# Optimization experiments

Measured on AMD Instinct MI355X. Metric: run time of the kernel, lower is better.

## Reference

```python
import jax, jax.numpy as jnp
import numpy as np

DIM = 4096
N_HEADS = 32
N_KV_HEADS = 8
HEAD_DIM = DIM // N_HEADS  # 128
N_REP = N_HEADS // N_KV_HEADS  # 4
MAX_BS = 16
MAX_SEQ = 4096
SEQLEN = 1
START_POS = 4095
ROPE_THETA = 500000.0


def setup_inputs() -> dict:
    key = jax.random.key(0)
    ks = jax.random.split(key, 8)
    w_scale = 0.02  # keep logits in a sane range
    x = jax.random.normal(ks[0], (MAX_BS, SEQLEN, DIM), dtype=jnp.float32)
    wq = jax.random.normal(ks[1], (DIM, N_HEADS * HEAD_DIM), dtype=jnp.float32) * w_scale
    wk = jax.random.normal(ks[2], (DIM, N_KV_HEADS * HEAD_DIM), dtype=jnp.float32) * w_scale
    wv = jax.random.normal(ks[3], (DIM, N_KV_HEADS * HEAD_DIM), dtype=jnp.float32) * w_scale
    wo = jax.random.normal(ks[4], (N_HEADS * HEAD_DIM, DIM), dtype=jnp.float32) * w_scale
    cache_k = jax.random.normal(ks[5], (MAX_BS, MAX_SEQ, N_KV_HEADS, HEAD_DIM), dtype=jnp.float32)
    cache_v = jax.random.normal(ks[6], (MAX_BS, MAX_SEQ, N_KV_HEADS, HEAD_DIM), dtype=jnp.float32)
    # true rotary frequencies for positions [START_POS, START_POS+SEQLEN)
    inv_freq = 1.0 / (ROPE_THETA ** (np.arange(0, HEAD_DIM, 2, dtype=np.float32) / HEAD_DIM))  # [hd/2]
    t = np.arange(START_POS, START_POS + SEQLEN, dtype=np.float32)[:, None]  # [s,1]
    angles = t * inv_freq[None, :]  # [s, hd/2]
    freqs_cos = jnp.asarray(np.cos(angles), dtype=jnp.float32)
    freqs_sin = jnp.asarray(np.sin(angles), dtype=jnp.float32)
    return {"x": x, "wq": wq, "wk": wk, "wv": wv, "wo": wo,
            "cache_k": cache_k, "cache_v": cache_v,
            "freqs_cos": freqs_cos, "freqs_sin": freqs_sin,
            "start_pos": START_POS}


def _rope(t, cos, sin):
    # t: [b, s, h, hd]; cos/sin: [s, hd/2] -> broadcast [1, s, 1, hd/2]
    b, s, h, hd = t.shape
    tp = t.reshape(b, s, h, hd // 2, 2)
    e, o = tp[..., 0], tp[..., 1]
    c = cos[None, :, None, :]
    sn = sin[None, :, None, :]
    re = e * c - o * sn
    im = e * sn + o * c
    return jnp.stack([re, im], axis=-1).reshape(b, s, h, hd)


def reference(x, wq, wk, wv, wo, cache_k, cache_v, freqs_cos, freqs_sin, start_pos):
    bsz, seqlen, _ = x.shape
    xq = (x @ wq).reshape(bsz, seqlen, N_HEADS, HEAD_DIM)
    xk = (x @ wk).reshape(bsz, seqlen, N_KV_HEADS, HEAD_DIM)
    xv = (x @ wv).reshape(bsz, seqlen, N_KV_HEADS, HEAD_DIM)
    xq = _rope(xq, freqs_cos, freqs_sin)
    xk = _rope(xk, freqs_cos, freqs_sin)
    # KV-cache append
    cache_k = jax.lax.dynamic_update_slice(cache_k, xk, (0, start_pos, 0, 0))
    cache_v = jax.lax.dynamic_update_slice(cache_v, xv, (0, start_pos, 0, 0))
    kv_len = start_pos + seqlen  # static Python int
    keys = cache_k[:, :kv_len]    # [b, t, g, hd]
    values = cache_v[:, :kv_len]  # [b, t, g, hd]
    # GQA via broadcasting (math-equivalent to repeat_kv)
    q = xq.reshape(bsz, seqlen, N_KV_HEADS, N_REP, HEAD_DIM)
    scale = 1.0 / jnp.sqrt(jnp.float32(HEAD_DIM))
    scores = jnp.einsum('bsgrh,btgh->bgrst', q, keys) * scale  # [b,g,r,s,t]
    probs = jax.nn.softmax(scores.astype(jnp.float32), axis=-1).astype(xq.dtype)
    out = jnp.einsum('bgrst,btgh->bsgrh', probs, values)  # [b,s,g,r,hd]
    out = out.reshape(bsz, seqlen, N_HEADS * HEAD_DIM)
    return out @ wo
```

## Files before the change

### kernel.cpp

```cpp
#include <hip/hip_runtime.h>
#include <math.h>

#define DIM    4096
#define NH     32
#define NKV    8
#define HD     128
#define BS     16
#define KVLEN  4096
#define LASTPOS 4095
#define QKV_COLS 6144

#define WS_QKV   0
#define WS_ATTN  98304
#define WS_PART  163840

__global__ __launch_bounds__(256) void qkv_proj(
    const float* __restrict__ x, const float* __restrict__ wq,
    const float* __restrict__ wk, const float* __restrict__ wv,
    float* __restrict__ qkv) {
  __shared__ float xs[16 * 128];
  const int tid = threadIdx.x;
  const int col = (blockIdx.x * 256 + tid) * 2;
  const int k0 = blockIdx.y * 128;

  for (int i = tid; i < 2048; i += 256) {
    int b = i >> 7, k = i & 127;
    xs[i] = x[b * DIM + k0 + k];
  }
  __syncthreads();

  const float* w;
  int wstride, wcol;
  if (col < 4096)      { w = wq; wstride = 4096; wcol = col; }
  else if (col < 5120) { w = wk; wstride = 1024; wcol = col - 4096; }
  else                 { w = wv; wstride = 1024; wcol = col - 5120; }
  const float* wp = w + (size_t)k0 * wstride + wcol;

  float acc0[16], acc1[16];
#pragma unroll
  for (int b = 0; b < 16; ++b) { acc0[b] = 0.f; acc1[b] = 0.f; }

  for (int k = 0; k < 128; k += 4) {
    float2 w0 = *(const float2*)(wp + (size_t)(k + 0) * wstride);
    float2 w1 = *(const float2*)(wp + (size_t)(k + 1) * wstride);
    float2 w2 = *(const float2*)(wp + (size_t)(k + 2) * wstride);
    float2 w3 = *(const float2*)(wp + (size_t)(k + 3) * wstride);
#pragma unroll
    for (int b = 0; b < 16; ++b) {
      float4 xb = *(const float4*)(&xs[b * 128 + k]);
      acc0[b] += xb.x * w0.x + xb.y * w1.x + xb.z * w2.x + xb.w * w3.x;
      acc1[b] += xb.x * w0.y + xb.y * w1.y + xb.z * w2.y + xb.w * w3.y;
    }
  }
#pragma unroll
  for (int b = 0; b < 16; ++b) {
    atomicAdd(&qkv[b * QKV_COLS + col],     acc0[b]);
    atomicAdd(&qkv[b * QKV_COLS + col + 1], acc1[b]);
  }
}

__global__ __launch_bounds__(256) void rope_kernel(
    float* __restrict__ qkv, const float* __restrict__ fc,
    const float* __restrict__ fs) {
  int t = blockIdx.x * 256 + threadIdx.x;
  if (t >= 16 * 40 * 64) return;
  int i  = t & 63;
  int hh = (t >> 6) % 40;
  int b  = t / (40 * 64);
  float c = fc[i], s = fs[i];
  int base;
  float scale;
  if (hh < 32) { base = b * QKV_COLS + hh * 128 + 2 * i; scale = 0.08838834764831845f; }
  else         { base = b * QKV_COLS + 4096 + (hh - 32) * 128 + 2 * i; scale = 1.0f; }
  float e = qkv[base], o = qkv[base + 1];
  qkv[base]     = (e * c - o * s) * scale;
  qkv[base + 1] = (e * s + o * c) * scale;
}

__global__ __launch_bounds__(512, 4) void attn_partial(
    const float* __restrict__ cache_k, const float* __restrict__ cache_v,
    const float* __restrict__ qkv, float* __restrict__ part) {
  __shared__ float qs[512];
  __shared__ float ss[4 * 512];
  __shared__ float pacc[8][4][128];
  const int tid = threadIdx.x;
  const int w = tid >> 6, lane = tid & 63;
  const int p = lane >> 4, ql = lane & 15;
  const int chunk = blockIdx.x & 7;
  const int bg = blockIdx.x >> 3;
  const int b = bg >> 3, g = bg & 7;

  qs[tid & 511] = qkv[b * QKV_COLS + g * 512 + (tid & 511)];
  __syncthreads();

  float4 qA[4], qB[4];
#pragma unroll
  for (int h = 0; h < 4; ++h) {
    qA[h] = *(const float4*)(&qs[h * 128 + ql * 8]);
    qB[h] = *(const float4*)(&qs[h * 128 + ql * 8 + 4]);
  }

  const int t0 = chunk * 512;
  const float* kbase = cache_k + ((size_t)b * 4096 * 8 + g) * 128;
  const float* xk    = qkv + b * QKV_COLS + 4096 + g * 128;

  for (int it = 0; it < 16; ++it) {
    int r = w * 64 + it * 4 + p;
    int t = t0 + r;
    const float* krow = (t == LASTPOS) ? xk : (kbase + (size_t)t * 1024);
    float4 k0 = *(const float4*)(krow + ql * 8);
    float4 k1 = *(const float4*)(krow + ql * 8 + 4);
    float s[4];
#pragma unroll
    for (int h = 0; h < 4; ++h) {
      s[h] = k0.x * qA[h].x + k0.y * qA[h].y + k0.z * qA[h].z + k0.w * qA[h].w
           + k1.x * qB[h].x + k1.y * qB[h].y + k1.z * qB[h].z + k1.w * qB[h].w;
    }
#pragma unroll
    for (int off = 1; off < 16; off <<= 1) {
#pragma unroll
      for (int h = 0; h < 4; ++h) s[h] += __shfl_xor(s[h], off);
    }
    float v = (ql == 0) ? s[0] : (ql == 1) ? s[1] : (ql == 2) ? s[2] : s[3];
    if (ql < 4) ss[ql * 512 + r] = v;
  }
  __syncthreads();

  float* prow = part + ((size_t)(bg * 8 + chunk) * 4 + (w & 3)) * 130;
  if (w < 4) {
    float vals[8];
    float m = -1e30f;
#pragma unroll
    for (int i = 0; i < 8; ++i) {
      vals[i] = ss[w * 512 + lane + 64 * i];
      m = fmaxf(m, vals[i]);
    }
#pragma unroll
    for (int off = 1; off < 64; off <<= 1) m = fmaxf(m, __shfl_xor(m, off));
    float l = 0.f;
#pragma unroll
    for (int i = 0; i < 8; ++i) {
      float pe = __expf(vals[i] - m);
      ss[w * 512 + lane + 64 * i] = pe;
      l += pe;
    }
#pragma unroll
    for (int off = 1; off < 64; off <<= 1) l += __shfl_xor(l, off);
    if (lane == 0) { prow[128] = m; prow[129] = l; }
  }
  __syncthreads();

  const float* vbase = cache_v + ((size_t)b * 4096 * 8 + g) * 128;
  const float* xv    = qkv + b * QKV_COLS + 5120 + g * 128;
  float ax[4] = {0.f, 0.f, 0.f, 0.f}, ay[4] = {0.f, 0.f, 0.f, 0.f};
  for (int j = 0; j < 64; ++j) {
    int r = w * 64 + j;
    int t = t0 + r;
    const float* vrow = (t == LASTPOS) ? xv : (vbase + (size_t)t * 1024);
    float2 vv = ((const float2*)vrow)[lane];
    float p0 = ss[0 * 512 + r];
    float p1 = ss[1 * 512 + r];
    float p2 = ss[2 * 512 + r];
    float p3 = ss[3 * 512 + r];
    ax[0] += p0 * vv.x; ay[0] += p0 * vv.y;
    ax[1] += p1 * vv.x; ay[1] += p1 * vv.y;
    ax[2] += p2 * vv.x; ay[2] += p2 * vv.y;
    ax[3] += p3 * vv.x; ay[3] += p3 * vv.y;
  }
#pragma unroll
  for (int h = 0; h < 4; ++h) {
    pacc[w][h][2 * lane]     = ax[h];
    pacc[w][h][2 * lane + 1] = ay[h];
  }
  __syncthreads();

  {
    int h = tid >> 7, d = tid & 127;
    float sum = 0.f;
#pragma unroll
    for (int w2 = 0; w2 < 8; ++w2) sum += pacc[w2][h][d];
    part[((size_t)(bg * 8 + chunk) * 4 + h) * 130 + d] = sum;
  }
}

__global__ __launch_bounds__(256) void attn_combine(
    const float* __restrict__ part, float* __restrict__ attn_out) {
  int t = blockIdx.x * 256 + threadIdx.x;
  int d = t & 127, r = (t >> 7) & 3, bg = t >> 9;
  int b = bg >> 3, g = bg & 7;
  float ms[8];
  float M = -1e30f;
#pragma unroll
  for (int c = 0; c < 8; ++c) {
    ms[c] = part[((size_t)(bg * 8 + c) * 4 + r) * 130 + 128];
    M = fmaxf(M, ms[c]);
  }
  float num = 0.f, den = 0.f;
#pragma unroll
  for (int c = 0; c < 8; ++c) {
    const float* prow = part + ((size_t)(bg * 8 + c) * 4 + r) * 130;
    float wgt = __expf(ms[c] - M);
    num += wgt * prow[d];
    den += wgt * prow[129];
  }
  attn_out[b * DIM + (g * 4 + r) * 128 + d] = num / den;
}

__global__ __launch_bounds__(256) void out_proj(
    const float* __restrict__ attn, const float* __restrict__ wo,
    float* __restrict__ out) {
  __shared__ float xs[16 * 128];
  const int tid = threadIdx.x;
  const int col = (blockIdx.x * 256 + tid) * 2;
  const int k0 = blockIdx.y * 128;

  for (int i = tid; i < 2048; i += 256) {
    int b = i >> 7, k = i & 127;
    xs[i] = attn[b * DIM + k0 + k];
  }
  __syncthreads();

  const float* wp = wo + (size_t)k0 * 4096 + col;
  float acc0[16], acc1[16];
#pragma unroll
  for (int b = 0; b < 16; ++b) { acc0[b] = 0.f; acc1[b] = 0.f; }

  for (int k = 0; k < 128; k += 4) {
    float2 w0 = *(const float2*)(wp + (size_t)(k + 0) * 4096);
    float2 w1 = *(const float2*)(wp + (size_t)(k + 1) * 4096);
    float2 w2 = *(const float2*)(wp + (size_t)(k + 2) * 4096);
    float2 w3 = *(const float2*)(wp + (size_t)(k + 3) * 4096);
#pragma unroll
    for (int b = 0; b < 16; ++b) {
      float4 xb = *(const float4*)(&xs[b * 128 + k]);
      acc0[b] += xb.x * w0.x + xb.y * w1.x + xb.z * w2.x + xb.w * w3.x;
      acc1[b] += xb.x * w0.y + xb.y * w1.y + xb.z * w2.y + xb.w * w3.y;
    }
  }
#pragma unroll
  for (int b = 0; b < 16; ++b) {
    atomicAdd(&out[b * DIM + col],     acc0[b]);
    atomicAdd(&out[b * DIM + col + 1], acc1[b]);
  }
}

extern "C" void kernel_launch(void* const* d_in, const int* in_sizes, int n_in,
                              void* d_out, int out_size, void* d_ws, size_t ws_size,
                              hipStream_t stream) {
  const float* x  = (const float*)d_in[0];
  const float* wq = (const float*)d_in[1];
  const float* wk = (const float*)d_in[2];
  const float* wv = (const float*)d_in[3];
  const float* wo = (const float*)d_in[4];
  const float* ck = (const float*)d_in[5];
  const float* cv = (const float*)d_in[6];
  const float* fc = (const float*)d_in[7];
  const float* fs = (const float*)d_in[8];

  float* ws_f  = (float*)d_ws;
  float* qkv   = ws_f + WS_QKV;
  float* attn  = ws_f + WS_ATTN;
  float* part  = ws_f + WS_PART;
  float* out   = (float*)d_out;

  hipMemsetAsync(qkv, 0, 98304 * sizeof(float), stream);
  hipMemsetAsync(out, 0, 65536 * sizeof(float), stream);

  qkv_proj<<<dim3(12, 32), 256, 0, stream>>>(x, wq, wk, wv, qkv);
  rope_kernel<<<160, 256, 0, stream>>>(qkv, fc, fs);
  attn_partial<<<1024, 512, 0, stream>>>(ck, cv, qkv, part);
  attn_combine<<<256, 256, 0, stream>>>(part, attn);
  out_proj<<<dim3(8, 32), 256, 0, stream>>>(attn, wo, out);
}
```

Before: 202.3 us.

## Split GEMV K-dimension finer, widen V loads, pad score smem, fuse memsets

The QKV and output projections now split K into 64-wide slices, doubling the block count, and the output projection gives each thread one column instead of two. This raises parallelism for the weight-streaming GEMVs at the cost of twice as many atomicAdds. In attention, the P·V loop loads float4 V rows with two rows per wave iteration and reduces halves via shuffle, and the score buffer gets a padded stride to avoid LDS bank conflicts. The two hipMemsetAsync calls are replaced by a single zeroing kernel.

```diff
diff --git a/kernel.cpp b/kernel.cpp
--- a/kernel.cpp
+++ b/kernel.cpp
@@ -9,22 +9,31 @@
 #define KVLEN  4096
 #define LASTPOS 4095
 #define QKV_COLS 6144
+#define SS_STR 520
 
 #define WS_QKV   0
 #define WS_ATTN  98304
 #define WS_PART  163840
+
+__global__ __launch_bounds__(256) void zero_ws(
+    float* __restrict__ qkv, float* __restrict__ out) {
+  int i = blockIdx.x * 256 + threadIdx.x;
+  float4 z = make_float4(0.f, 0.f, 0.f, 0.f);
+  if (i < 24576) ((float4*)qkv)[i] = z;
+  else           ((float4*)out)[i - 24576] = z;
+}
 
 __global__ __launch_bounds__(256) void qkv_proj(
     const float* __restrict__ x, const float* __restrict__ wq,
     const float* __restrict__ wk, const float* __restrict__ wv,
     float* __restrict__ qkv) {
-  __shared__ float xs[16 * 128];
+  __shared__ float xs[16 * 64];
   const int tid = threadIdx.x;
   const int col = (blockIdx.x * 256 + tid) * 2;
-  const int k0 = blockIdx.y * 128;
-
-  for (int i = tid; i < 2048; i += 256) {
-    int b = i >> 7, k = i & 127;
+  const int k0 = blockIdx.y * 64;
+
+  for (int i = tid; i < 1024; i += 256) {
+    int b = i >> 6, k = i & 63;
     xs[i] = x[b * DIM + k0 + k];
   }
   __syncthreads();
@@ -40,14 +49,15 @@
 #pragma unroll
   for (int b = 0; b < 16; ++b) { acc0[b] = 0.f; acc1[b] = 0.f; }
 
-  for (int k = 0; k < 128; k += 4) {
+#pragma unroll 2
+  for (int k = 0; k < 64; k += 4) {
     float2 w0 = *(const float2*)(wp + (size_t)(k + 0) * wstride);
     float2 w1 = *(const float2*)(wp + (size_t)(k + 1) * wstride);
     float2 w2 = *(const float2*)(wp + (size_t)(k + 2) * wstride);
     float2 w3 = *(const float2*)(wp + (size_t)(k + 3) * wstride);
 #pragma unroll
     for (int b = 0; b < 16; ++b) {
-      float4 xb = *(const float4*)(&xs[b * 128 + k]);
+      float4 xb = *(const float4*)(&xs[b * 64 + k]);
       acc0[b] += xb.x * w0.x + xb.y * w1.x + xb.z * w2.x + xb.w * w3.x;
       acc1[b] += xb.x * w0.y + xb.y * w1.y + xb.z * w2.y + xb.w * w3.y;
     }
@@ -81,7 +91,7 @@
     const float* __restrict__ cache_k, const float* __restrict__ cache_v,
     const float* __restrict__ qkv, float* __restrict__ part) {
   __shared__ float qs[512];
-  __shared__ float ss[4 * 512];
+  __shared__ float ss[4 * SS_STR];
   __shared__ float pacc[8][4][128];
   const int tid = threadIdx.x;
   const int w = tid >> 6, lane = tid & 63;
@@ -90,7 +100,7 @@
   const int bg = blockIdx.x >> 3;
   const int b = bg >> 3, g = bg & 7;
 
-  qs[tid & 511] = qkv[b * QKV_COLS + g * 512 + (tid & 511)];
+  qs[tid] = qkv[b * QKV_COLS + g * 512 + tid];
   __syncthreads();
 
   float4 qA[4], qB[4];
@@ -122,7 +132,7 @@
       for (int h = 0; h < 4; ++h) s[h] += __shfl_xor(s[h], off);
     }
     float v = (ql == 0) ? s[0] : (ql == 1) ? s[1] : (ql == 2) ? s[2] : s[3];
-    if (ql < 4) ss[ql * 512 + r] = v;
+    if (ql < 4) ss[ql * SS_STR + r] = v;
   }
   __syncthreads();
 
@@ -132,7 +142,7 @@
     float m = -1e30f;
 #pragma unroll
     for (int i = 0; i < 8; ++i) {
-      vals[i] = ss[w * 512 + lane + 64 * i];
+      vals[i] = ss[w * SS_STR + lane + 64 * i];
       m = fmaxf(m, vals[i]);
     }
 #pragma unroll
@@ -141,7 +151,7 @@
 #pragma unroll
     for (int i = 0; i < 8; ++i) {
       float pe = __expf(vals[i] - m);
-      ss[w * 512 + lane + 64 * i] = pe;
+      ss[w * SS_STR + lane + 64 * i] = pe;
       l += pe;
     }
 #pragma unroll
@@ -152,25 +162,38 @@
 
   const float* vbase = cache_v + ((size_t)b * 4096 * 8 + g) * 128;
   const float* xv    = qkv + b * QKV_COLS + 5120 + g * 128;
-  float ax[4] = {0.f, 0.f, 0.f, 0.f}, ay[4] = {0.f, 0.f, 0.f, 0.f};
-  for (int j = 0; j < 64; ++j) {
-    int r = w * 64 + j;
+  const int h2 = lane >> 5;
+  const int dq = lane & 31;
+  float4 acc[4];
+#pragma unroll
+  for (int h = 0; h < 4; ++h) acc[h] = make_float4(0.f, 0.f, 0.f, 0.f);
+
+#pragma unroll 2
+  for (int j = 0; j < 32; ++j) {
+    int r = w * 64 + 2 * j + h2;
     int t = t0 + r;
     const float* vrow = (t == LASTPOS) ? xv : (vbase + (size_t)t * 1024);
-    float2 vv = ((const float2*)vrow)[lane];
-    float p0 = ss[0 * 512 + r];
-    float p1 = ss[1 * 512 + r];
-    float p2 = ss[2 * 512 + r];
-    float p3 = ss[3 * 512 + r];
-    ax[0] += p0 * vv.x; ay[0] += p0 * vv.y;
-    ax[1] += p1 * vv.x; ay[1] += p1 * vv.y;
-    ax[2] += p2 * vv.x; ay[2] += p2 * vv.y;
-    ax[3] += p3 * vv.x; ay[3] += p3 * vv.y;
+    float4 vv = *(const float4*)(vrow + dq * 4);
+    float p0 = ss[0 * SS_STR + r];
+    float p1 = ss[1 * SS_STR + r];
+    float p2 = ss[2 * SS_STR + r];
+    float p3 = ss[3 * SS_STR + r];
+    acc[0].x += p0 * vv.x; acc[0].y += p0 * vv.y; acc[0].z += p0 * vv.z; acc[0].w += p0 * vv.w;
+    acc[1].x += p1 * vv.x; acc[1].y += p1 * vv.y; acc[1].z += p1 * vv.z; acc[1].w += p1 * vv.w;
+    acc[2].x += p2 * vv.x; acc[2].y += p2 * vv.y; acc[2].z += p2 * vv.z; acc[2].w += p2 * vv.w;
+    acc[3].x += p3 * vv.x; acc[3].y += p3 * vv.y; acc[3].z += p3 * vv.z; acc[3].w += p3 * vv.w;
   }
 #pragma unroll
   for (int h = 0; h < 4; ++h) {
-    pacc[w][h][2 * lane]     = ax[h];
-    pacc[w][h][2 * lane + 1] = ay[h];
+    acc[h].x += __shfl_xor(acc[h].x, 32);
+    acc[h].y += __shfl_xor(acc[h].y, 32);
+    acc[h].z += __shfl_xor(acc[h].z, 32);
+    acc[h].w += __shfl_xor(acc[h].w, 32);
+  }
+  if (lane < 32) {
+#pragma unroll
+    for (int h = 0; h < 4; ++h)
+      *(float4*)(&pacc[w][h][dq * 4]) = acc[h];
   }
   __syncthreads();
 
@@ -209,39 +232,36 @@
 __global__ __launch_bounds__(256) void out_proj(
     const float* __restrict__ attn, const float* __restrict__ wo,
     float* __restrict__ out) {
-  __shared__ float xs[16 * 128];
+  __shared__ float xs[16 * 64];
   const int tid = threadIdx.x;
-  const int col = (blockIdx.x * 256 + tid) * 2;
-  const int k0 = blockIdx.y * 128;
-
-  for (int i = tid; i < 2048; i += 256) {
-    int b = i >> 7, k = i & 127;
+  const int col = blockIdx.x * 256 + tid;
+  const int k0 = blockIdx.y * 64;
+
+  for (int i = tid; i < 1024; i += 256) {
+    int b = i >> 6, k = i & 63;
     xs[i] = attn[b * DIM + k0 + k];
   }
   __syncthreads();
 
   const float* wp = wo + (size_t)k0 * 4096 + col;
-  float acc0[16], acc1[16];
-#pragma unroll
-  for (int b = 0; b < 16; ++b) { acc0[b] = 0.f; acc1[b] = 0.f; }
-
-  for (int k = 0; k < 128; k += 4) {
-    float2 w0 = *(const float2*)(wp + (size_t)(k + 0) * 4096);
-    float2 w1 = *(const float2*)(wp + (size_t)(k + 1) * 4096);
-    float2 w2 = *(const float2*)(wp + (size_t)(k + 2) * 4096);
-    float2 w3 = *(const float2*)(wp + (size_t)(k + 3) * 4096);
+  float acc[16];
+#pragma unroll
+  for (int b = 0; b < 16; ++b) acc[b] = 0.f;
+
+#pragma unroll 2
+  for (int k = 0; k < 64; k += 4) {
+    float w0 = wp[(size_t)(k + 0) * 4096];
+    float w1 = wp[(size_t)(k + 1) * 4096];
+    float w2 = wp[(size_t)(k + 2) * 4096];
+    float w3 = wp[(size_t)(k + 3) * 4096];
 #pragma unroll
     for (int b = 0; b < 16; ++b) {
-      float4 xb = *(const float4*)(&xs[b * 128 + k]);
-      acc0[b] += xb.x * w0.x + xb.y * w1.x + xb.z * w2.x + xb.w * w3.x;
-      acc1[b] += xb.x * w0.y + xb.y * w1.y + xb.z * w2.y + xb.w * w3.y;
-    }
-  }
-#pragma unroll
-  for (int b = 0; b < 16; ++b) {
-    atomicAdd(&out[b * DIM + col],     acc0[b]);
-    atomicAdd(&out[b * DIM + col + 1], acc1[b]);
-  }
+      float4 xb = *(const float4*)(&xs[b * 64 + k]);
+      acc[b] += xb.x * w0 + xb.y * w1 + xb.z * w2 + xb.w * w3;
+    }
+  }
+#pragma unroll
+  for (int b = 0; b < 16; ++b) atomicAdd(&out[b * DIM + col], acc[b]);
 }
 
 extern "C" void kernel_launch(void* const* d_in, const int* in_sizes, int n_in,
@@ -263,12 +283,10 @@
   float* part  = ws_f + WS_PART;
   float* out   = (float*)d_out;
 
-  hipMemsetAsync(qkv, 0, 98304 * sizeof(float), stream);
-  hipMemsetAsync(out, 0, 65536 * sizeof(float), stream);
-
-  qkv_proj<<<dim3(12, 32), 256, 0, stream>>>(x, wq, wk, wv, qkv);
+  zero_ws<<<160, 256, 0, stream>>>(qkv, out);
+  qkv_proj<<<dim3(12, 64), 256, 0, stream>>>(x, wq, wk, wv, qkv);
   rope_kernel<<<160, 256, 0, stream>>>(qkv, fc, fs);
   attn_partial<<<1024, 512, 0, stream>>>(ck, cv, qkv, part);
   attn_combine<<<256, 256, 0, stream>>>(part, attn);
-  out_proj<<<dim3(8, 32), 256, 0, stream>>>(attn, wo, out);
-}
+  out_proj<<<dim3(16, 64), 256, 0, stream>>>(attn, wo, out);
+}
```

Result: no change. 202.8 us (+0.2%).
